# Optimization experiments

Measured on AMD Instinct MI355X. Metric: run time of the kernel, lower is better.

Reference implementation:

```python
import jax, jax.numpy as jnp
import numpy as np

NEIGHBOR_NUM = 32  # init kwarg neighbor_num

B, N, C = 64, 512, 1024

def setup_inputs() -> dict:
    key = jax.random.key(0)
    x = jax.random.normal(key, (B, N, C), dtype=jnp.float32)
    return {"x": x}

def reference(x):
    # si = x @ x^T (detached in the original -> stop_gradient)
    si = jax.lax.stop_gradient(x)
    si = jnp.einsum('bic,bjc->bij', si, si)  # (b, n, n)
    # k-th largest value per row as threshold
    topv, _ = jax.lax.top_k(si, NEIGHBOR_NUM)          # (b, n, k)
    threshold = topv[..., -1:]                          # (b, n, 1)
    adj = (si >= threshold).astype(si.dtype)            # (b, n, n)
    # normalize_digraph: D^{-1/2} A D^{-1/2} with D = row-degree diag
    node_degrees = adj.sum(axis=-1)                     # (b, n)
    degs_inv_sqrt = node_degrees ** (-0.5)              # (b, n)
    # diag(d) @ A @ diag(d) == d_i * A_ij * d_j
    norm_A = degs_inv_sqrt[:, :, None] * adj * degs_inv_sqrt[:, None, :]
    return norm_A
```

## Files before the change

### kernel.cpp

```cpp
#include <hip/hip_runtime.h>
#include <hip/hip_bf16.h>
#include <math.h>

#define B 64
#define N 512
#define C 1024
#define K_NEIGH 32
#define DELTA 0.9f
#define BISECT_ITERS 12

typedef __attribute__((ext_vector_type(8))) _Float16 half8;
typedef __attribute__((ext_vector_type(4))) float f32x4;

__device__ __forceinline__ half8 cvt8(float4 a, float4 b) {
    half8 g;
    g[0] = (_Float16)a.x; g[1] = (_Float16)a.y; g[2] = (_Float16)a.z; g[3] = (_Float16)a.w;
    g[4] = (_Float16)b.x; g[5] = (_Float16)b.y; g[6] = (_Float16)b.z; g[7] = (_Float16)b.w;
    return g;
}

__global__ __launch_bounds__(512, 2) void gemm_f16(const float* __restrict__ x,
                                                   _Float16* __restrict__ S16) {
    __shared__ half8 Ah[2][1024];
    __shared__ half8 Bh[2][1024];

    const int id   = blockIdx.x;
    const int xcd  = id & 7;
    const int slot = id >> 3;
    const int b    = xcd * 8 + (slot >> 2);
    const int tile = slot & 3;
    const int ti = tile >> 1, tj = tile & 1;
    const int row0 = ti * 256;
    const int col0 = tj * 256;
    const float* xb = x + (size_t)b * N * C;
    const bool diag = (ti == tj);

    const int t    = threadIdx.x;
    const int w    = t >> 6;
    const int lane = t & 63;
    const int quad = lane >> 4;
    const int lid  = lane & 15;
    const int wr   = (w >> 2) * 128;
    const int wc   = (w & 3) * 64;

    const int srow = t >> 1;
    const int s0   = (t & 1) * 2;
    const int koff = (t & 1) * 16;

    f32x4 acc[8][4];
#pragma unroll
    for (int r = 0; r < 8; r++)
#pragma unroll
        for (int c = 0; c < 4; c++)
#pragma unroll
            for (int e = 0; e < 4; e++) acc[r][c][e] = 0.f;

    const float* pArow = xb + (size_t)(row0 + srow) * C + koff;
    const float* pBrow = xb + (size_t)(col0 + srow) * C + koff;

    float4 ra[4], rb[4];
    {
        const float4* pa = (const float4*)pArow;
#pragma unroll
        for (int i = 0; i < 4; i++) ra[i] = pa[i];
        if (!diag) {
            const float4* pb = (const float4*)pBrow;
#pragma unroll
            for (int i = 0; i < 4; i++) rb[i] = pb[i];
        }
    }

    const int NIT = C / 32;
    for (int it = 0; it < NIT; ++it) {
        const int p = it & 1;
        Ah[p][s0 * 256 + srow]       = cvt8(ra[0], ra[1]);
        Ah[p][(s0 + 1) * 256 + srow] = cvt8(ra[2], ra[3]);
        if (!diag) {
            Bh[p][s0 * 256 + srow]       = cvt8(rb[0], rb[1]);
            Bh[p][(s0 + 1) * 256 + srow] = cvt8(rb[2], rb[3]);
        }
        if (it + 1 < NIT) {
            const float4* pa = (const float4*)(pArow + (it + 1) * 32);
#pragma unroll
            for (int i = 0; i < 4; i++) ra[i] = pa[i];
            if (!diag) {
                const float4* pb = (const float4*)(pBrow + (it + 1) * 32);
#pragma unroll
                for (int i = 0; i < 4; i++) rb[i] = pb[i];
            }
        }
        asm volatile("s_waitcnt lgkmcnt(0)" ::: "memory");
        __builtin_amdgcn_s_barrier();
        const half8* Ab = &Ah[p][0];
        const half8* Bb = diag ? Ab : &Bh[p][0];
        half8 vb[4];
#pragma unroll
        for (int c = 0; c < 4; c++) vb[c] = Bb[quad * 256 + wc + c * 16 + lid];
        __builtin_amdgcn_s_setprio(1);
#pragma unroll
        for (int r = 0; r < 8; r++) {
            half8 va = Ab[quad * 256 + wr + r * 16 + lid];
#pragma unroll
            for (int c = 0; c < 4; c++)
                acc[r][c] = __builtin_amdgcn_mfma_f32_16x16x32_f16(va, vb[c], acc[r][c], 0, 0, 0);
        }
        __builtin_amdgcn_s_setprio(0);
    }

    _Float16* Sb = S16 + (size_t)b * N * N;
#pragma unroll
    for (int r = 0; r < 8; r++) {
#pragma unroll
        for (int c = 0; c < 4; c++) {
#pragma unroll
            for (int e = 0; e < 4; e++) {
                const int grow = row0 + wr + r * 16 + quad * 4 + e;
                const int gcol = col0 + wc + c * 16 + lid;
                Sb[(size_t)grow * N + gcol] = (_Float16)acc[r][c][e];
            }
        }
    }
}

__global__ __launch_bounds__(256) void thresh_mask(const _Float16* __restrict__ S16,
                                                   const float* __restrict__ x,
                                                   unsigned long long* __restrict__ masks,
                                                   float* __restrict__ dinv) {
    const int id   = blockIdx.x;
    const int xcd  = id & 7;
    const int slot = id >> 3;
    const int bsw  = xcd * 8 + (slot >> 7);
    const int rblk = slot & 127;
    const int row  = bsw * N + rblk * 4 + (threadIdx.x >> 6);
    const int lane = threadIdx.x & 63;
    const _Float16* Srow = S16 + (size_t)row * N;

    float v0[8];
#pragma unroll
    for (int k = 0; k < 8; k++) v0[k] = (float)Srow[lane + 64 * k];

    float lo = -1400.f, hi = 1400.f;
    for (int it = 0; it < BISECT_ITERS; it++) {
        const float mid = 0.5f * (lo + hi);
        int c = 0;
#pragma unroll
        for (int k = 0; k < 8; k++) c += __popcll(__ballot(v0[k] > mid));
        if (c >= K_NEIGH) lo = mid; else hi = mid;
    }
    const float P   = 0.5f * (lo + hi);
    const float hiB = P + DELTA, loB = P - DELTA;

    int cA = 0;
#pragma unroll
    for (int k = 0; k < 8; k++) cA += __popcll(__ballot(v0[k] > hiB));
    const int m_need = K_NEIGH - cA;

    int cnt = 0, myj = -1;
#pragma unroll
    for (int kq = 0; kq < 8; kq++) {
        unsigned long long bm = __ballot(v0[kq] >= loB && v0[kq] <= hiB);
        while (bm) {
            int bl = __ffsll(bm) - 1;
            bm &= bm - 1;
            if (cnt == lane) myj = bl + 64 * kq;
            cnt++;
        }
    }
    const int nc = cnt < 64 ? cnt : 64;

    const int bb_ = row >> 9, ii = row & (N - 1);
    const float* xi = x + ((size_t)bb_ * N + ii) * C;
    float4 ai[4];
#pragma unroll
    for (int q = 0; q < 4; q++) ai[q] = *(const float4*)(xi + q * 256 + lane * 4);

    float ex = -INFINITY;
    for (int c2 = 0; c2 < nc; c2++) {
        const int j = __shfl(myj, c2);
        const float* xj = x + ((size_t)bb_ * N + j) * C;
        float s = 0.f;
#pragma unroll
        for (int q = 0; q < 4; q++) {
            float4 bv = *(const float4*)(xj + q * 256 + lane * 4);
            s = fmaf(ai[q].x, bv.x, s);
            s = fmaf(ai[q].y, bv.y, s);
            s = fmaf(ai[q].z, bv.z, s);
            s = fmaf(ai[q].w, bv.w, s);
        }
#pragma unroll
        for (int off = 32; off > 0; off >>= 1) s += __shfl_xor(s, off);
        if (lane == c2) ex = s;
    }

    float val = ex, T = -INFINITY;
    for (int it = 0; it < m_need; it++) {
        float M = val;
#pragma unroll
        for (int off = 32; off > 0; off >>= 1) M = fmaxf(M, __shfl_xor(M, off));
        T = M;
        unsigned long long ball = __ballot(val == M);
        int first = __ffsll(ball) - 1;
        if (lane == first) val = -INFINITY;
    }
    const int dec = (lane < nc && ex >= T) ? 1 : 0;

    int bits[8];
#pragma unroll
    for (int kq = 0; kq < 8; kq++) bits[kq] = (v0[kq] > hiB) ? 1 : 0;
    for (int c2 = 0; c2 < nc; c2++) {
        int j = __shfl(myj, c2);
        int d = __shfl(dec, c2);
        if ((j & 63) == lane) bits[j >> 6] = d;
    }

    unsigned long long msk[8];
    int deg = 0;
#pragma unroll
    for (int kq = 0; kq < 8; kq++) {
        msk[kq] = __ballot(bits[kq] != 0);
        deg += __popcll(msk[kq]);
    }
    if (lane == 0) {
#pragma unroll
        for (int kq = 0; kq < 8; kq++) masks[(size_t)row * 8 + kq] = msk[kq];
        dinv[row] = rsqrtf((float)deg);
    }
}

__global__ __launch_bounds__(256) void scale_adj(float* __restrict__ Sout,
                                                 const unsigned long long* __restrict__ masks,
                                                 const float* __restrict__ dinv) {
    const int idx = blockIdx.x * 256 + threadIdx.x;
    const int jq = idx & 127;
    const int i  = (idx >> 7) & (N - 1);
    const int b  = idx >> 16;
    const int row = (b << 9) | i;
    const int j0 = jq * 4;

    const unsigned long long mk = masks[(size_t)row * 8 + (j0 >> 6)];
    const float di = dinv[row];
    float4 dj = ((const float4*)dinv)[(b << 7) | jq];

    float4 o;
    o.x = ((mk >> ((j0 + 0) & 63)) & 1ull) ? di * dj.x : 0.f;
    o.y = ((mk >> ((j0 + 1) & 63)) & 1ull) ? di * dj.y : 0.f;
    o.z = ((mk >> ((j0 + 2) & 63)) & 1ull) ? di * dj.z : 0.f;
    o.w = ((mk >> ((j0 + 3) & 63)) & 1ull) ? di * dj.w : 0.f;
    ((float4*)Sout)[idx] = o;
}

extern "C" void kernel_launch(void* const* d_in, const int* in_sizes, int n_in,
                              void* d_out, int out_size, void* d_ws, size_t ws_size,
                              hipStream_t stream) {
    const float* x = (const float*)d_in[0];
    float* out = (float*)d_out;
    _Float16* S16 = (_Float16*)d_out;
    unsigned long long* masks = (unsigned long long*)d_ws;
    float* dinv = (float*)(masks + (size_t)B * N * 8);

    gemm_f16<<<dim3(B * 4), 512, 0, stream>>>(x, S16);
    thresh_mask<<<B * N / 4, 256, 0, stream>>>(S16, x, masks, dinv);
    const int total4 = B * N * N / 4;
    scale_adj<<<total4 / 256, 256, 0, stream>>>(out, masks, dinv);
}
```

Before: 271.2 us.

## Fuse GEMM with threshold selection via shared-memory strips and seeded bisection

Merges the f16 GEMM and the threshold/mask kernel. Each block now computes a 128x512 row strip of the similarity matrix and keeps it in shared memory, so the f16 matrix is never written to or read back from global memory. It also adds a statistical estimate of the k-th value (an RMS-based guess) to narrow the bisection range to fewer iterations when the estimate brackets correctly. In exchange, each block stages all 512 rows of x per K step, the serial per-row thresholding runs inside the GEMM blocks with only 256 blocks, and the large shared-memory union limits occupancy.

```diff
diff --git a/kernel.cpp b/kernel.cpp
--- a/kernel.cpp
+++ b/kernel.cpp
@@ -19,211 +19,199 @@
     return g;
 }
 
-__global__ __launch_bounds__(512, 2) void gemm_f16(const float* __restrict__ x,
-                                                   _Float16* __restrict__ S16) {
-    __shared__ half8 Ah[2][1024];
-    __shared__ half8 Bh[2][1024];
-
-    const int id   = blockIdx.x;
-    const int xcd  = id & 7;
-    const int slot = id >> 3;
-    const int b    = xcd * 8 + (slot >> 2);
-    const int tile = slot & 3;
-    const int ti = tile >> 1, tj = tile & 1;
-    const int row0 = ti * 256;
-    const int col0 = tj * 256;
+__global__ __launch_bounds__(512, 2) void gemm_thresh(const float* __restrict__ x,
+                                                      unsigned long long* __restrict__ masks,
+                                                      float* __restrict__ dinv) {
+    __shared__ union {
+        half8    Bst[2][2048];
+        _Float16 S[128][512];
+    } sh;
+
+    const int id    = blockIdx.x;
+    const int xcd   = id & 7;
+    const int slot  = id >> 3;
+    const int b     = xcd * 8 + (slot >> 2);
+    const int strip = slot & 3;
+    const int row0  = strip * 128;
     const float* xb = x + (size_t)b * N * C;
-    const bool diag = (ti == tj);
 
     const int t    = threadIdx.x;
     const int w    = t >> 6;
     const int lane = t & 63;
     const int quad = lane >> 4;
     const int lid  = lane & 15;
-    const int wr   = (w >> 2) * 128;
-    const int wc   = (w & 3) * 64;
-
-    const int srow = t >> 1;
-    const int s0   = (t & 1) * 2;
-    const int koff = (t & 1) * 16;
-
-    f32x4 acc[8][4];
-#pragma unroll
-    for (int r = 0; r < 8; r++)
-#pragma unroll
-        for (int c = 0; c < 4; c++)
+    const int wr   = (w >> 2) * 64;
+    const int wc   = (w & 3) * 128;
+
+    f32x4 acc[4][8];
+#pragma unroll
+    for (int r = 0; r < 4; r++)
+#pragma unroll
+        for (int c = 0; c < 8; c++)
 #pragma unroll
             for (int e = 0; e < 4; e++) acc[r][c][e] = 0.f;
 
-    const float* pArow = xb + (size_t)(row0 + srow) * C + koff;
-    const float* pBrow = xb + (size_t)(col0 + srow) * C + koff;
-
-    float4 ra[4], rb[4];
-    {
-        const float4* pa = (const float4*)pArow;
-#pragma unroll
-        for (int i = 0; i < 4; i++) ra[i] = pa[i];
-        if (!diag) {
-            const float4* pb = (const float4*)pBrow;
-#pragma unroll
-            for (int i = 0; i < 4; i++) rb[i] = pb[i];
-        }
-    }
+    const float* prow = xb + (size_t)t * C;
+
+    float4 rx[8];
+#pragma unroll
+    for (int i = 0; i < 8; i++) rx[i] = ((const float4*)prow)[i];
 
     const int NIT = C / 32;
     for (int it = 0; it < NIT; ++it) {
         const int p = it & 1;
-        Ah[p][s0 * 256 + srow]       = cvt8(ra[0], ra[1]);
-        Ah[p][(s0 + 1) * 256 + srow] = cvt8(ra[2], ra[3]);
-        if (!diag) {
-            Bh[p][s0 * 256 + srow]       = cvt8(rb[0], rb[1]);
-            Bh[p][(s0 + 1) * 256 + srow] = cvt8(rb[2], rb[3]);
-        }
+#pragma unroll
+        for (int s = 0; s < 4; s++)
+            sh.Bst[p][s * 512 + t] = cvt8(rx[2 * s], rx[2 * s + 1]);
         if (it + 1 < NIT) {
-            const float4* pa = (const float4*)(pArow + (it + 1) * 32);
-#pragma unroll
-            for (int i = 0; i < 4; i++) ra[i] = pa[i];
-            if (!diag) {
-                const float4* pb = (const float4*)(pBrow + (it + 1) * 32);
-#pragma unroll
-                for (int i = 0; i < 4; i++) rb[i] = pb[i];
-            }
+            const float4* pp = (const float4*)(prow + (it + 1) * 32);
+#pragma unroll
+            for (int i = 0; i < 8; i++) rx[i] = pp[i];
         }
         asm volatile("s_waitcnt lgkmcnt(0)" ::: "memory");
         __builtin_amdgcn_s_barrier();
-        const half8* Ab = &Ah[p][0];
-        const half8* Bb = diag ? Ab : &Bh[p][0];
-        half8 vb[4];
-#pragma unroll
-        for (int c = 0; c < 4; c++) vb[c] = Bb[quad * 256 + wc + c * 16 + lid];
+        const half8* Bb = &sh.Bst[p][0];
+        half8 va[4];
+#pragma unroll
+        for (int r = 0; r < 4; r++) va[r] = Bb[quad * 512 + row0 + wr + r * 16 + lid];
         __builtin_amdgcn_s_setprio(1);
 #pragma unroll
-        for (int r = 0; r < 8; r++) {
-            half8 va = Ab[quad * 256 + wr + r * 16 + lid];
-#pragma unroll
-            for (int c = 0; c < 4; c++)
-                acc[r][c] = __builtin_amdgcn_mfma_f32_16x16x32_f16(va, vb[c], acc[r][c], 0, 0, 0);
+        for (int c = 0; c < 8; c++) {
+            half8 vb = Bb[quad * 512 + wc + c * 16 + lid];
+#pragma unroll
+            for (int r = 0; r < 4; r++)
+                acc[r][c] = __builtin_amdgcn_mfma_f32_16x16x32_f16(va[r], vb, acc[r][c], 0, 0, 0);
         }
         __builtin_amdgcn_s_setprio(0);
     }
 
-    _Float16* Sb = S16 + (size_t)b * N * N;
-#pragma unroll
-    for (int r = 0; r < 8; r++) {
-#pragma unroll
-        for (int c = 0; c < 4; c++) {
-#pragma unroll
-            for (int e = 0; e < 4; e++) {
-                const int grow = row0 + wr + r * 16 + quad * 4 + e;
-                const int gcol = col0 + wc + c * 16 + lid;
-                Sb[(size_t)grow * N + gcol] = (_Float16)acc[r][c][e];
+    __syncthreads();
+#pragma unroll
+    for (int r = 0; r < 4; r++)
+#pragma unroll
+        for (int c = 0; c < 8; c++)
+#pragma unroll
+            for (int e = 0; e < 4; e++)
+                sh.S[wr + r * 16 + quad * 4 + e][wc + c * 16 + lid] = (_Float16)acc[r][c][e];
+    __syncthreads();
+
+    for (int rr = 0; rr < 16; ++rr) {
+        const int lr   = w * 16 + rr;
+        const int gi   = row0 + lr;
+        const int grow = b * N + gi;
+
+        float v0[8];
+#pragma unroll
+        for (int k = 0; k < 8; k++) v0[k] = (float)sh.S[lr][lane + 64 * k];
+
+        const float* xi = x + ((size_t)b * N + gi) * C;
+        float4 ai[4];
+#pragma unroll
+        for (int q = 0; q < 4; q++) ai[q] = *(const float4*)(xi + q * 256 + lane * 4);
+
+        float sum2 = 0.f;
+#pragma unroll
+        for (int k = 0; k < 8; k++) {
+            const float v = ((lane + 64 * k) == gi) ? 0.f : v0[k];
+            sum2 = fmaf(v, v, sum2);
+        }
+#pragma unroll
+        for (int off = 32; off > 0; off >>= 1) sum2 += __shfl_xor(sum2, off);
+        const float Pest = 1.542f * sqrtf(sum2 * (1.0f / 511.0f));
+        const float bhi = Pest + 10.f, blo = Pest - 10.f;
+        int chk_hi = 0, chk_lo = 0;
+#pragma unroll
+        for (int k = 0; k < 8; k++) {
+            chk_hi += __popcll(__ballot(v0[k] > bhi));
+            chk_lo += __popcll(__ballot(v0[k] > blo));
+        }
+
+        float lo, hi;
+        int nit;
+        if (chk_hi <= K_NEIGH - 1 && chk_lo >= K_NEIGH) {
+            lo = blo; hi = bhi; nit = 5;
+        } else {
+            lo = -1400.f; hi = 1400.f; nit = BISECT_ITERS;
+        }
+        for (int i2 = 0; i2 < nit; i2++) {
+            const float mid = 0.5f * (lo + hi);
+            int cc = 0;
+#pragma unroll
+            for (int k = 0; k < 8; k++) cc += __popcll(__ballot(v0[k] > mid));
+            if (cc >= K_NEIGH) lo = mid; else hi = mid;
+        }
+        const float P   = 0.5f * (lo + hi);
+        const float hiB = P + DELTA, loB = P - DELTA;
+
+        int cA = 0;
+#pragma unroll
+        for (int k = 0; k < 8; k++) cA += __popcll(__ballot(v0[k] > hiB));
+        const int m_need = K_NEIGH - cA;
+
+        int cnt = 0, myj = -1;
+#pragma unroll
+        for (int kq = 0; kq < 8; kq++) {
+            unsigned long long bm = __ballot(v0[kq] >= loB && v0[kq] <= hiB);
+            while (bm) {
+                int bl = __ffsll(bm) - 1;
+                bm &= bm - 1;
+                if (cnt == lane) myj = bl + 64 * kq;
+                cnt++;
             }
         }
-    }
-}
-
-__global__ __launch_bounds__(256) void thresh_mask(const _Float16* __restrict__ S16,
-                                                   const float* __restrict__ x,
-                                                   unsigned long long* __restrict__ masks,
-                                                   float* __restrict__ dinv) {
-    const int id   = blockIdx.x;
-    const int xcd  = id & 7;
-    const int slot = id >> 3;
-    const int bsw  = xcd * 8 + (slot >> 7);
-    const int rblk = slot & 127;
-    const int row  = bsw * N + rblk * 4 + (threadIdx.x >> 6);
-    const int lane = threadIdx.x & 63;
-    const _Float16* Srow = S16 + (size_t)row * N;
-
-    float v0[8];
-#pragma unroll
-    for (int k = 0; k < 8; k++) v0[k] = (float)Srow[lane + 64 * k];
-
-    float lo = -1400.f, hi = 1400.f;
-    for (int it = 0; it < BISECT_ITERS; it++) {
-        const float mid = 0.5f * (lo + hi);
-        int c = 0;
-#pragma unroll
-        for (int k = 0; k < 8; k++) c += __popcll(__ballot(v0[k] > mid));
-        if (c >= K_NEIGH) lo = mid; else hi = mid;
-    }
-    const float P   = 0.5f * (lo + hi);
-    const float hiB = P + DELTA, loB = P - DELTA;
-
-    int cA = 0;
-#pragma unroll
-    for (int k = 0; k < 8; k++) cA += __popcll(__ballot(v0[k] > hiB));
-    const int m_need = K_NEIGH - cA;
-
-    int cnt = 0, myj = -1;
-#pragma unroll
-    for (int kq = 0; kq < 8; kq++) {
-        unsigned long long bm = __ballot(v0[kq] >= loB && v0[kq] <= hiB);
-        while (bm) {
-            int bl = __ffsll(bm) - 1;
-            bm &= bm - 1;
-            if (cnt == lane) myj = bl + 64 * kq;
-            cnt++;
-        }
-    }
-    const int nc = cnt < 64 ? cnt : 64;
-
-    const int bb_ = row >> 9, ii = row & (N - 1);
-    const float* xi = x + ((size_t)bb_ * N + ii) * C;
-    float4 ai[4];
-#pragma unroll
-    for (int q = 0; q < 4; q++) ai[q] = *(const float4*)(xi + q * 256 + lane * 4);
-
-    float ex = -INFINITY;
-    for (int c2 = 0; c2 < nc; c2++) {
-        const int j = __shfl(myj, c2);
-        const float* xj = x + ((size_t)bb_ * N + j) * C;
-        float s = 0.f;
-#pragma unroll
-        for (int q = 0; q < 4; q++) {
-            float4 bv = *(const float4*)(xj + q * 256 + lane * 4);
-            s = fmaf(ai[q].x, bv.x, s);
-            s = fmaf(ai[q].y, bv.y, s);
-            s = fmaf(ai[q].z, bv.z, s);
-            s = fmaf(ai[q].w, bv.w, s);
-        }
-#pragma unroll
-        for (int off = 32; off > 0; off >>= 1) s += __shfl_xor(s, off);
-        if (lane == c2) ex = s;
-    }
-
-    float val = ex, T = -INFINITY;
-    for (int it = 0; it < m_need; it++) {
-        float M = val;
-#pragma unroll
-        for (int off = 32; off > 0; off >>= 1) M = fmaxf(M, __shfl_xor(M, off));
-        T = M;
-        unsigned long long ball = __ballot(val == M);
-        int first = __ffsll(ball) - 1;
-        if (lane == first) val = -INFINITY;
-    }
-    const int dec = (lane < nc && ex >= T) ? 1 : 0;
-
-    int bits[8];
-#pragma unroll
-    for (int kq = 0; kq < 8; kq++) bits[kq] = (v0[kq] > hiB) ? 1 : 0;
-    for (int c2 = 0; c2 < nc; c2++) {
-        int j = __shfl(myj, c2);
-        int d = __shfl(dec, c2);
-        if ((j & 63) == lane) bits[j >> 6] = d;
-    }
-
-    unsigned long long msk[8];
-    int deg = 0;
-#pragma unroll
-    for (int kq = 0; kq < 8; kq++) {
-        msk[kq] = __ballot(bits[kq] != 0);
-        deg += __popcll(msk[kq]);
-    }
-    if (lane == 0) {
-#pragma unroll
-        for (int kq = 0; kq < 8; kq++) masks[(size_t)row * 8 + kq] = msk[kq];
-        dinv[row] = rsqrtf((float)deg);
+        const int nc = cnt < 64 ? cnt : 64;
+
+        float ex = -INFINITY;
+        for (int c2 = 0; c2 < nc; c2++) {
+            const int j = __shfl(myj, c2);
+            const float* xj = x + ((size_t)b * N + j) * C;
+            float s = 0.f;
+#pragma unroll
+            for (int q = 0; q < 4; q++) {
+                float4 bv = *(const float4*)(xj + q * 256 + lane * 4);
+                s = fmaf(ai[q].x, bv.x, s);
+                s = fmaf(ai[q].y, bv.y, s);
+                s = fmaf(ai[q].z, bv.z, s);
+                s = fmaf(ai[q].w, bv.w, s);
+            }
+#pragma unroll
+            for (int off = 32; off > 0; off >>= 1) s += __shfl_xor(s, off);
+            if (lane == c2) ex = s;
+        }
+
+        float val = ex, T = -INFINITY;
+        for (int i2 = 0; i2 < m_need; i2++) {
+            float M = val;
+#pragma unroll
+            for (int off = 32; off > 0; off >>= 1) M = fmaxf(M, __shfl_xor(M, off));
+            T = M;
+            unsigned long long ball = __ballot(val == M);
+            int first = __ffsll(ball) - 1;
+            if (lane == first) val = -INFINITY;
+        }
+        const int dec = (lane < nc && ex >= T) ? 1 : 0;
+
+        int bits[8];
+#pragma unroll
+        for (int kq = 0; kq < 8; kq++) bits[kq] = (v0[kq] > hiB) ? 1 : 0;
+        for (int c2 = 0; c2 < nc; c2++) {
+            int j = __shfl(myj, c2);
+            int d = __shfl(dec, c2);
+            if ((j & 63) == lane) bits[j >> 6] = d;
+        }
+
+        unsigned long long msk[8];
+        int deg = 0;
+#pragma unroll
+        for (int kq = 0; kq < 8; kq++) {
+            msk[kq] = __ballot(bits[kq] != 0);
+            deg += __popcll(msk[kq]);
+        }
+        if (lane == 0) {
+#pragma unroll
+            for (int kq = 0; kq < 8; kq++) masks[(size_t)grow * 8 + kq] = msk[kq];
+            dinv[grow] = rsqrtf((float)deg);
+        }
     }
 }
 
@@ -254,12 +242,10 @@
                               hipStream_t stream) {
     const float* x = (const float*)d_in[0];
     float* out = (float*)d_out;
-    _Float16* S16 = (_Float16*)d_out;
     unsigned long long* masks = (unsigned long long*)d_ws;
     float* dinv = (float*)(masks + (size_t)B * N * 8);
 
-    gemm_f16<<<dim3(B * 4), 512, 0, stream>>>(x, S16);
-    thresh_mask<<<B * N / 4, 256, 0, stream>>>(S16, x, masks, dinv);
+    gemm_thresh<<<dim3(B * 4), 512, 0, stream>>>(x, masks, dinv);
     const int total4 = B * N * N / 4;
     scale_adj<<<total4 / 256, 256, 0, stream>>>(out, masks, dinv);
 }
```

New measurement: 373.9 us. 1.38x slower.
